# Kernel tuning notes

Measured on AMD Instinct MI355X. Metric: run time of the kernel, lower is better.

The kernel has to match this reference:

```python
import jax, jax.numpy as jnp
import numpy as np

# Module config (matches init_kwargs)
B, H, W, C = 2, 64, 64, 128
NH, K = 4, 7            # num_heads, kernel_size (odd)
HD = C // NH            # head_dim = 32
SCALE = HD ** -0.5


def setup_inputs() -> dict:
    key = jax.random.key(0)
    ks = jax.random.split(key, 5)
    return {
        "x": jax.random.normal(ks[0], (B, H, W, C), jnp.float32),
        "w_qkv": jax.random.normal(ks[1], (C, 3 * C), jnp.float32) * 0.02,
        "b_qkv": jnp.zeros((3 * C,), jnp.float32),
        "rpb": jax.random.normal(ks[2], (NH, 2 * K - 1, 2 * K - 1), jnp.float32) * 0.02,
        "w_proj": jax.random.normal(ks[3], (C, C), jnp.float32) * 0.02,
        "b_proj": jnp.zeros((C,), jnp.float32),
    }


def _window_starts(L):
    # NATTEN clamped window start: max(i-k//2,0), shifted left at right border so the
    # full k-window fits. clip handles both cases since i-k//2 > L-k  <=>  i+k//2 >= L.
    i = jnp.arange(L)
    return jnp.clip(i - K // 2, 0, L - K)  # [L]


def reference(x, w_qkv, b_qkv, rpb, w_proj, b_proj):
    # qkv projection: [B,H,W,3,NH,HD]
    qkv = (x @ w_qkv + b_qkv).reshape(B, H, W, 3, NH, HD)
    q = qkv[..., 0, :, :] * SCALE  # [B,H,W,NH,HD]
    k = qkv[..., 1, :, :]
    v = qkv[..., 2, :, :]

    a = jnp.arange(K)
    idx_h = _window_starts(H)[:, None] + a[None, :]  # [H,K] key rows per query row
    idx_w = _window_starts(W)[:, None] + a[None, :]  # [W,K] key cols per query col

    # Gather k*k neighborhoods (honors the local sparsity; no [HW,HW] matrix):
    # k[:, idx_h] -> [B,H,K,W,NH,HD]; then index W axis -> [B,H,K,W,K,NH,HD]
    k_nb = k[:, idx_h][:, :, :, idx_w]
    v_nb = v[:, idx_h][:, :, :, idx_w]

    # natten2dqkrpb: attn[b,n,i,j,p,q] = <q[b,i,j,n], k[b, ih[i,p], iw[j,q], n]>
    attn = jnp.einsum('bhwnd,bhpwqnd->bnhwpq', q, k_nb)  # [B,NH,H,W,K,K]

    # relative position bias index = (neighbor - query) + (k-1) per axis
    bidx_h = idx_h - jnp.arange(H)[:, None] + (K - 1)  # [H,K] in [0, 2k-2]
    bidx_w = idx_w - jnp.arange(W)[:, None] + (K - 1)  # [W,K]
    bias = rpb[:, bidx_h[:, :, None, None], bidx_w[None, None]]  # [NH,H,K,W,K]
    attn = attn + bias.transpose(0, 1, 3, 2, 4)[None]  # -> [1,NH,H,W,K,K]

    # softmax over the flattened k*k neighborhood
    attn = jax.nn.softmax(attn.reshape(B, NH, H, W, K * K), axis=-1)
    attn = attn.reshape(B, NH, H, W, K, K)

    # natten2dav: weighted sum over neighborhood values
    out = jnp.einsum('bnhwpq,bhpwqnd->bhwnd', attn, v_nb).reshape(B, H, W, C)
    return out @ w_proj + b_proj
```

## Files before the change

### kernel.cpp

```cpp
#include <hip/hip_runtime.h>
#include <hip/hip_bf16.h>
#include <cstddef>

#define BB 2
#define HH 64
#define WW 64
#define SCALE 0.17677669529663687f

#define HALO_H 10
#define HALO_W 14
#define NPIX 140
#define NQ 32

typedef short short8 __attribute__((ext_vector_type(8)));
typedef float f32x4 __attribute__((ext_vector_type(4)));

#if defined(__has_builtin)
#if __has_builtin(__builtin_amdgcn_fdot2_f32_bf16)
#define HAS_BFDOT2 1
#endif
#endif
#ifndef HAS_BFDOT2
#define HAS_BFDOT2 0
#endif

#if HAS_BFDOT2
typedef __bf16 v2bf __attribute__((ext_vector_type(2)));
__device__ inline float bfdot2(uint a, uint b, float c) {
    union { uint u; v2bf v; } ua, ub;
    ua.u = a; ub.u = b;
    return __builtin_amdgcn_fdot2_f32_bf16(ua.v, ub.v, c, false);
}
#endif

__device__ inline ushort f2bf(float f) {
    union { __hip_bfloat16 b; ushort u; } cv;
    cv.b = __float2bfloat16(f);
    return cv.u;
}
__device__ inline float bflo(uint u) { union { uint i; float f; } c; c.i = u << 16; return c.f; }
__device__ inline float bfhi(uint u) { union { uint i; float f; } c; c.i = u & 0xffff0000u; return c.f; }

__global__ __launch_bounds__(256) void qkv_gemm_fused_kernel(
    const float* __restrict__ x, const float* __restrict__ w_qkv,
    const float* __restrict__ b_qkv, const float* __restrict__ w_proj,
    ushort* __restrict__ qkv, ushort* __restrict__ Wp_t)
{
    __shared__ ushort S[64 * 128 + 96 * 128];
    ushort* As = S;
    ushort* Bs = S + 64 * 128;

    const int tid = threadIdx.x;
    const int m0 = blockIdx.x * 64;
    const int n0 = blockIdx.y * 96;

    if (blockIdx.y == 0 && tid < 128)
        Wp_t[(size_t)blockIdx.x * 128 + tid] =
            f2bf(w_proj[(size_t)tid * 128 + blockIdx.x]);

    #pragma unroll
    for (int t = 0; t < 4; ++t) {
        int idx = tid + t * 256;
        int r = idx >> 4, c = idx & 15;
        const float* src = x + (size_t)(m0 + r) * 128 + c * 8;
        float4 v0 = *(const float4*)src;
        float4 v1 = *(const float4*)(src + 4);
        union { ushort s[8]; uint4 q; } u;
        u.s[0] = f2bf(v0.x); u.s[1] = f2bf(v0.y); u.s[2] = f2bf(v0.z); u.s[3] = f2bf(v0.w);
        u.s[4] = f2bf(v1.x); u.s[5] = f2bf(v1.y); u.s[6] = f2bf(v1.z); u.s[7] = f2bf(v1.w);
        *(uint4*)&As[r * 128 + (c ^ (r & 7)) * 8] = u.q;
    }
    #pragma unroll
    for (int t = 0; t < 6; ++t) {
        int idx = tid + t * 256;
        int kc = idx / 96, n = idx - kc * 96;
        union { ushort s[8]; uint4 q; } u;
        #pragma unroll
        for (int e = 0; e < 8; ++e)
            u.s[e] = f2bf(w_qkv[(size_t)(kc * 8 + e) * 384 + n0 + n]);
        *(uint4*)&Bs[n * 128 + ((kc ^ (n & 7)) * 8)] = u.q;
    }
    __syncthreads();

    const int wid = tid >> 6, lane = tid & 63;
    const int l15 = lane & 15, l4 = lane >> 4;
    const int mr = (wid >> 1) * 32, nr = (wid & 1) * 48;

    f32x4 acc[2][3] = {};
    #pragma unroll
    for (int ks = 0; ks < 4; ++ks) {
        short8 af[2], bf[3];
        #pragma unroll
        for (int fm = 0; fm < 2; ++fm) {
            int row = mr + fm * 16 + l15;
            af[fm] = *(const short8*)&As[row * 128 + ((ks * 4 + l4) ^ (row & 7)) * 8];
        }
        #pragma unroll
        for (int fn = 0; fn < 3; ++fn) {
            int row = nr + fn * 16 + l15;
            bf[fn] = *(const short8*)&Bs[row * 128 + ((ks * 4 + l4) ^ (row & 7)) * 8];
        }
        #pragma unroll
        for (int fm = 0; fm < 2; ++fm)
            #pragma unroll
            for (int fn = 0; fn < 3; ++fn)
                acc[fm][fn] = __builtin_amdgcn_mfma_f32_16x16x32_bf16(
                    af[fm], bf[fn], acc[fm][fn], 0, 0, 0);
    }

    __syncthreads();
    ushort* C_s = S;
    #pragma unroll
    for (int fn = 0; fn < 3; ++fn) {
        int colb = nr + fn * 16;
        int col = colb + l15;
        float bc = b_qkv[n0 + col];
        float sc = (n0 + colb < 128) ? SCALE : 1.0f;
        #pragma unroll
        for (int fm = 0; fm < 2; ++fm)
            #pragma unroll
            for (int reg = 0; reg < 4; ++reg) {
                int row = mr + fm * 16 + l4 * 4 + reg;
                C_s[row * 200 + col] = f2bf((acc[fm][fn][reg] + bc) * sc);
            }
    }
    __syncthreads();
    #pragma unroll
    for (int t = 0; t < 3; ++t) {
        int idx = tid + t * 256;
        int row = idx / 12, c = idx - row * 12;
        uint4 v = *(const uint4*)&C_s[row * 200 + c * 8];
        *(uint4*)&qkv[(size_t)(m0 + row) * 384 + n0 + c * 8] = v;
    }
}

__global__ __launch_bounds__(256) void natten_proj_kernel(
    const ushort* __restrict__ qkv,
    const float* __restrict__ rpb,
    const ushort* __restrict__ Wp_t,
    const float* __restrict__ b_proj,
    float* __restrict__ out)
{
    __shared__ ushort KV_s[NPIX * 64];
    __shared__ ushort AO_s[NQ * 128];
    __shared__ float attn_s[NQ * 52];
    __shared__ float rpb_s[676];

    const int tid = threadIdx.x;
    const int bx = ((blockIdx.x & 7) << 5) | (blockIdx.x >> 3);
    const int b  = bx >> 7;
    const int th = (bx >> 3) & 15;
    const int tw = bx & 7;
    const int h0 = th * 4, w0 = tw * 8;
    const int ho = max(0, h0 - 3), wo = max(0, w0 - 3);

    #pragma unroll
    for (int t = 0; t < 3; ++t) {
        int idx = tid + t * 256;
        if (idx < 676) rpb_s[idx] = rpb[idx];
    }

    const int q = tid >> 3, t8 = tid & 7;
    const int qh = h0 + (q >> 3), qw = w0 + (q & 7);
    const int hs = min(max(qh - 3, 0), HH - 7);
    const int ws = min(max(qw - 3, 0), WW - 7);
    const int base_lp = (hs - ho) * HALO_W + (ws - wo);
    const int bh0 = hs - qh + 6, bw0 = ws - qw + 6;
    const size_t qpix = (size_t)((b << 12) + (qh << 6) + qw);

    for (int hd = 0; hd < 4; ++hd) {
        #pragma unroll
        for (int t = 0; t < 5; ++t) {
            int idx = tid + t * 256;
            if (idx < NPIX * 8) {
                int pix = idx >> 3, s = idx & 7;
                int r = pix / HALO_W, c = pix - r * HALO_W;
                int gh = min(ho + r, HH - 1), gw = min(wo + c, WW - 1);
                const ushort* gp = qkv + (size_t)((b << 12) + (gh << 6) + gw) * 384
                                   + 128 + (s >> 2) * 128 + hd * 32 + (s & 3) * 8;
                uint4 v = *(const uint4*)gp;
                int bb = (pix >> 2) & 1;
                int slot = (2 * ((s & 3) ^ (pix & 3)) ^ bb) ^ (s >> 2);
                *(uint4*)&KV_s[pix * 64 + slot * 8] = v;
            }
        }

#if HAS_BFDOT2
        uint4 qb[4];
        #pragma unroll
        for (int d4 = 0; d4 < 4; ++d4)
            qb[d4] = *(const uint4*)(qkv + qpix * 384 + hd * 32 + d4 * 8);
#else
        float qf[32];
        #pragma unroll
        for (int d4 = 0; d4 < 4; ++d4) {
            uint4 qu = *(const uint4*)(qkv + qpix * 384 + hd * 32 + d4 * 8);
            qf[d4*8+0] = bflo(qu.x); qf[d4*8+1] = bfhi(qu.x);
            qf[d4*8+2] = bflo(qu.y); qf[d4*8+3] = bfhi(qu.y);
            qf[d4*8+4] = bflo(qu.z); qf[d4*8+5] = bfhi(qu.z);
            qf[d4*8+6] = bflo(qu.w); qf[d4*8+7] = bfhi(qu.w);
        }
#endif
        __syncthreads();

        float lg[7];
        #pragma unroll
        for (int i = 0; i < 7; ++i) {
            int j = t8 + i * 8;
            float s = -1e30f;
            if (j < 49) {
                int p = (j * 37) >> 8;
                int qq = j - p * 7;
                int lp = base_lp + p * HALO_W + qq;
                int bb = (lp >> 2) & 1;
                float a = 0.f;
                #pragma unroll
                for (int d4 = 0; d4 < 4; ++d4) {
                    uint4 ku = *(const uint4*)&KV_s[lp * 64 + ((2 * (d4 ^ (lp & 3)) ^ bb) * 8)];
#if HAS_BFDOT2
                    a = bfdot2(ku.x, qb[d4].x, a);
                    a = bfdot2(ku.y, qb[d4].y, a);
                    a = bfdot2(ku.z, qb[d4].z, a);
                    a = bfdot2(ku.w, qb[d4].w, a);
#else
                    a += bflo(ku.x)*qf[d4*8+0] + bfhi(ku.x)*qf[d4*8+1]
                       + bflo(ku.y)*qf[d4*8+2] + bfhi(ku.y)*qf[d4*8+3]
                       + bflo(ku.z)*qf[d4*8+4] + bfhi(ku.z)*qf[d4*8+5]
                       + bflo(ku.w)*qf[d4*8+6] + bfhi(ku.w)*qf[d4*8+7];
#endif
                }
                s = a + rpb_s[hd * 169 + (bh0 + p) * 13 + (bw0 + qq)];
            }
            lg[i] = s;
        }

        float m = lg[0];
        #pragma unroll
        for (int i = 1; i < 7; ++i) m = fmaxf(m, lg[i]);
        m = fmaxf(m, __shfl_xor(m, 1));
        m = fmaxf(m, __shfl_xor(m, 2));
        m = fmaxf(m, __shfl_xor(m, 4));
        float ssum = 0.f;
        #pragma unroll
        for (int i = 0; i < 7; ++i) {
            int j = t8 + i * 8;
            lg[i] = (j < 49) ? __expf(lg[i] - m) : 0.f;
            ssum += lg[i];
        }
        ssum += __shfl_xor(ssum, 1);
        ssum += __shfl_xor(ssum, 2);
        ssum += __shfl_xor(ssum, 4);
        float inv = 1.f / ssum;
        #pragma unroll
        for (int i = 0; i < 7; ++i) {
            int j = t8 + i * 8;
            if (j < 49) attn_s[q * 52 + j] = lg[i] * inv;
        }

        const int dd = t8 & 3;
        const int jp = t8 >> 2;
        float o[8] = {};
        #pragma unroll
        for (int i = 0; i < 25; ++i) {
            int j = 2 * i + jp;
            if (j < 49) {
                int p = (j * 37) >> 8;
                int qq = j - p * 7;
                int lp = base_lp + p * HALO_W + qq;
                int bb = (lp >> 2) & 1;
                float a = attn_s[q * 52 + j];
                uint4 vu = *(const uint4*)&KV_s[lp * 64 + (((2 * (dd ^ (lp & 3)) ^ bb) ^ 1) * 8)];
                o[0] += a * bflo(vu.x); o[1] += a * bfhi(vu.x);
                o[2] += a * bflo(vu.y); o[3] += a * bfhi(vu.y);
                o[4] += a * bflo(vu.z); o[5] += a * bfhi(vu.z);
                o[6] += a * bflo(vu.w); o[7] += a * bfhi(vu.w);
            }
        }
        #pragma unroll
        for (int e = 0; e < 8; ++e) o[e] += __shfl_xor(o[e], 4);

        if (t8 < 4) {
            union { ushort s[8]; uint4 u4; } w;
            #pragma unroll
            for (int e = 0; e < 8; ++e) w.s[e] = f2bf(o[e]);
            *(uint4*)&AO_s[q * 128 + (((hd * 4 + dd) ^ (q & 7)) * 8)] = w.u4;
        }
        __syncthreads();
    }

    const int wid = tid >> 6, lane = tid & 63;
    const int l15 = lane & 15, l4 = lane >> 4;
    const int wr = wid >> 1, wc = wid & 1;

    f32x4 pacc[4] = {};
    #pragma unroll
    for (int ks = 0; ks < 4; ++ks) {
        int arow = wr * 16 + l15;
        short8 af = *(const short8*)&AO_s[arow * 128 + ((ks * 4 + l4) ^ (arow & 7)) * 8];
        #pragma unroll
        for (int fn = 0; fn < 4; ++fn) {
            int brow = wc * 64 + fn * 16 + l15;
            short8 bf = *(const short8*)(Wp_t + (size_t)brow * 128 + (ks * 4 + l4) * 8);
            pacc[fn] = __builtin_amdgcn_mfma_f32_16x16x32_bf16(af, bf, pacc[fn], 0, 0, 0);
        }
    }
    #pragma unroll
    for (int fn = 0; fn < 4; ++fn) {
        int col = wc * 64 + fn * 16 + l15;
        float bc = b_proj[col];
        #pragma unroll
        for (int reg = 0; reg < 4; ++reg) {
            int q2 = wr * 16 + l4 * 4 + reg;
            int oh = h0 + (q2 >> 3), ow = w0 + (q2 & 7);
            out[(size_t)((b << 12) + (oh << 6) + ow) * 128 + col] = pacc[fn][reg] + bc;
        }
    }
}

extern "C" void kernel_launch(void* const* d_in, const int* in_sizes, int n_in,
                              void* d_out, int out_size, void* d_ws, size_t ws_size,
                              hipStream_t stream)
{
    const float* x      = (const float*)d_in[0];
    const float* w_qkv  = (const float*)d_in[1];
    const float* b_qkv  = (const float*)d_in[2];
    const float* rpb    = (const float*)d_in[3];
    const float* w_proj = (const float*)d_in[4];
    const float* b_proj = (const float*)d_in[5];
    float* out = (float*)d_out;

    const int M = BB * HH * WW;
    ushort* qkv  = (ushort*)d_ws;
    ushort* Wp_t = qkv + (size_t)M * 384;

    qkv_gemm_fused_kernel<<<dim3(128, 4), 256, 0, stream>>>(
        x, w_qkv, b_qkv, w_proj, qkv, Wp_t);

    natten_proj_kernel<<<256, 256, 0, stream>>>(
        qkv, rpb, Wp_t, b_proj, out);
}
```

Before: 30.33 us.

## Assign one head per wavefront with private K/V tiles, removing per-head block syncs

Replaces the serial loop over four heads, where the whole block reloaded a shared K/V halo and synchronised twice per head, with a layout in which each of the four wavefronts owns one head and its own K/V halo buffer. Each query is now handled by two lanes holding 25 logits in registers, so the attention-probability shared array and its round trip go away, and only one block barrier remains before the projection MFMA. This trades more shared memory (four halo buffers) and much higher register pressure (25 logits plus 32 accumulators per lane) for fewer barriers and more independent loads in flight, which may lower occupancy.

After: 30.34 us. Within noise of the previous version (+0.0%).

```diff
diff --git a/kernel.cpp b/kernel.cpp
--- a/kernel.cpp
+++ b/kernel.cpp
@@ -141,12 +141,13 @@
     const float* __restrict__ b_proj,
     float* __restrict__ out)
 {
-    __shared__ ushort KV_s[NPIX * 64];
+    __shared__ ushort KV_s[4][NPIX * 64];
     __shared__ ushort AO_s[NQ * 128];
-    __shared__ float attn_s[NQ * 52];
     __shared__ float rpb_s[676];
 
     const int tid = threadIdx.x;
+    const int wv = tid >> 6;
+    const int lane = tid & 63;
     const int bx = ((blockIdx.x & 7) << 5) | (blockIdx.x >> 3);
     const int b  = bx >> 7;
     const int th = (bx >> 3) & 15;
@@ -160,7 +161,24 @@
         if (idx < 676) rpb_s[idx] = rpb[idx];
     }
 
-    const int q = tid >> 3, t8 = tid & 7;
+    ushort* KV = &KV_s[wv][0];
+    #pragma unroll
+    for (int t = 0; t < 18; ++t) {
+        int idx = lane + t * 64;
+        if (idx < NPIX * 8) {
+            int pix = idx >> 3, s = idx & 7;
+            int r = pix / HALO_W, c = pix - r * HALO_W;
+            int gh = min(ho + r, HH - 1), gw = min(wo + c, WW - 1);
+            const ushort* gp = qkv + (size_t)((b << 12) + (gh << 6) + gw) * 384
+                               + 128 + (s >> 2) * 128 + wv * 32 + (s & 3) * 8;
+            uint4 v = *(const uint4*)gp;
+            int bb = (pix >> 2) & 1;
+            int slot = (2 * ((s & 3) ^ (pix & 3)) ^ bb) ^ (s >> 2);
+            *(uint4*)&KV[pix * 64 + slot * 8] = v;
+        }
+    }
+
+    const int q = lane >> 1, half = lane & 1;
     const int qh = h0 + (q >> 3), qw = w0 + (q & 7);
     const int hs = min(max(qh - 3, 0), HH - 7);
     const int ws = min(max(qw - 3, 0), WW - 7);
@@ -168,129 +186,106 @@
     const int bh0 = hs - qh + 6, bw0 = ws - qw + 6;
     const size_t qpix = (size_t)((b << 12) + (qh << 6) + qw);
 
-    for (int hd = 0; hd < 4; ++hd) {
-        #pragma unroll
-        for (int t = 0; t < 5; ++t) {
-            int idx = tid + t * 256;
-            if (idx < NPIX * 8) {
-                int pix = idx >> 3, s = idx & 7;
-                int r = pix / HALO_W, c = pix - r * HALO_W;
-                int gh = min(ho + r, HH - 1), gw = min(wo + c, WW - 1);
-                const ushort* gp = qkv + (size_t)((b << 12) + (gh << 6) + gw) * 384
-                                   + 128 + (s >> 2) * 128 + hd * 32 + (s & 3) * 8;
-                uint4 v = *(const uint4*)gp;
-                int bb = (pix >> 2) & 1;
-                int slot = (2 * ((s & 3) ^ (pix & 3)) ^ bb) ^ (s >> 2);
-                *(uint4*)&KV_s[pix * 64 + slot * 8] = v;
+#if HAS_BFDOT2
+    uint4 qb[4];
+    #pragma unroll
+    for (int d4 = 0; d4 < 4; ++d4)
+        qb[d4] = *(const uint4*)(qkv + qpix * 384 + wv * 32 + d4 * 8);
+#else
+    float qf[32];
+    #pragma unroll
+    for (int d4 = 0; d4 < 4; ++d4) {
+        uint4 qu = *(const uint4*)(qkv + qpix * 384 + wv * 32 + d4 * 8);
+        qf[d4*8+0] = bflo(qu.x); qf[d4*8+1] = bfhi(qu.x);
+        qf[d4*8+2] = bflo(qu.y); qf[d4*8+3] = bfhi(qu.y);
+        qf[d4*8+4] = bflo(qu.z); qf[d4*8+5] = bfhi(qu.z);
+        qf[d4*8+6] = bflo(qu.w); qf[d4*8+7] = bfhi(qu.w);
+    }
+#endif
+    __syncthreads();
+
+    float lg[25];
+    #pragma unroll
+    for (int i = 0; i < 25; ++i) {
+        int j = half + 2 * i;
+        float s = -1e30f;
+        if (j < 49) {
+            int p = (j * 37) >> 8;
+            int qq = j - p * 7;
+            int lp = base_lp + p * HALO_W + qq;
+            int bb = (lp >> 2) & 1;
+            float a = 0.f;
+            #pragma unroll
+            for (int d4 = 0; d4 < 4; ++d4) {
+                uint4 ku = *(const uint4*)&KV[lp * 64 + ((2 * (d4 ^ (lp & 3)) ^ bb) * 8)];
+#if HAS_BFDOT2
+                a = bfdot2(ku.x, qb[d4].x, a);
+                a = bfdot2(ku.y, qb[d4].y, a);
+                a = bfdot2(ku.z, qb[d4].z, a);
+                a = bfdot2(ku.w, qb[d4].w, a);
+#else
+                a += bflo(ku.x)*qf[d4*8+0] + bfhi(ku.x)*qf[d4*8+1]
+                   + bflo(ku.y)*qf[d4*8+2] + bfhi(ku.y)*qf[d4*8+3]
+                   + bflo(ku.z)*qf[d4*8+4] + bfhi(ku.z)*qf[d4*8+5]
+                   + bflo(ku.w)*qf[d4*8+6] + bfhi(ku.w)*qf[d4*8+7];
+#endif
             }
-        }
-
-#if HAS_BFDOT2
-        uint4 qb[4];
-        #pragma unroll
-        for (int d4 = 0; d4 < 4; ++d4)
-            qb[d4] = *(const uint4*)(qkv + qpix * 384 + hd * 32 + d4 * 8);
-#else
-        float qf[32];
-        #pragma unroll
-        for (int d4 = 0; d4 < 4; ++d4) {
-            uint4 qu = *(const uint4*)(qkv + qpix * 384 + hd * 32 + d4 * 8);
-            qf[d4*8+0] = bflo(qu.x); qf[d4*8+1] = bfhi(qu.x);
-            qf[d4*8+2] = bflo(qu.y); qf[d4*8+3] = bfhi(qu.y);
-            qf[d4*8+4] = bflo(qu.z); qf[d4*8+5] = bfhi(qu.z);
-            qf[d4*8+6] = bflo(qu.w); qf[d4*8+7] = bfhi(qu.w);
-        }
-#endif
-        __syncthreads();
-
-        float lg[7];
-        #pragma unroll
-        for (int i = 0; i < 7; ++i) {
-            int j = t8 + i * 8;
-            float s = -1e30f;
-            if (j < 49) {
-                int p = (j * 37) >> 8;
-                int qq = j - p * 7;
-                int lp = base_lp + p * HALO_W + qq;
-                int bb = (lp >> 2) & 1;
-                float a = 0.f;
-                #pragma unroll
-                for (int d4 = 0; d4 < 4; ++d4) {
-                    uint4 ku = *(const uint4*)&KV_s[lp * 64 + ((2 * (d4 ^ (lp & 3)) ^ bb) * 8)];
-#if HAS_BFDOT2
-                    a = bfdot2(ku.x, qb[d4].x, a);
-                    a = bfdot2(ku.y, qb[d4].y, a);
-                    a = bfdot2(ku.z, qb[d4].z, a);
-                    a = bfdot2(ku.w, qb[d4].w, a);
-#else
-                    a += bflo(ku.x)*qf[d4*8+0] + bfhi(ku.x)*qf[d4*8+1]
-                       + bflo(ku.y)*qf[d4*8+2] + bfhi(ku.y)*qf[d4*8+3]
-                       + bflo(ku.z)*qf[d4*8+4] + bfhi(ku.z)*qf[d4*8+5]
-                       + bflo(ku.w)*qf[d4*8+6] + bfhi(ku.w)*qf[d4*8+7];
-#endif
-                }
-                s = a + rpb_s[hd * 169 + (bh0 + p) * 13 + (bw0 + qq)];
+            s = a + rpb_s[wv * 169 + (bh0 + p) * 13 + (bw0 + qq)];
+        }
+        lg[i] = s;
+    }
+
+    float m = lg[0];
+    #pragma unroll
+    for (int i = 1; i < 25; ++i) m = fmaxf(m, lg[i]);
+    m = fmaxf(m, __shfl_xor(m, 1));
+    float ssum = 0.f;
+    #pragma unroll
+    for (int i = 0; i < 25; ++i) {
+        int j = half + 2 * i;
+        lg[i] = (j < 49) ? __expf(lg[i] - m) : 0.f;
+        ssum += lg[i];
+    }
+    ssum += __shfl_xor(ssum, 1);
+    float inv = 1.f / ssum;
+    #pragma unroll
+    for (int i = 0; i < 25; ++i) lg[i] *= inv;
+
+    float o[32] = {};
+    #pragma unroll
+    for (int i = 0; i < 25; ++i) {
+        int j = half + 2 * i;
+        if (j < 49) {
+            int p = (j * 37) >> 8;
+            int qq = j - p * 7;
+            int lp = base_lp + p * HALO_W + qq;
+            int bb = (lp >> 2) & 1;
+            float a = lg[i];
+            #pragma unroll
+            for (int d4 = 0; d4 < 4; ++d4) {
+                uint4 vu = *(const uint4*)&KV[lp * 64 + (((2 * (d4 ^ (lp & 3)) ^ bb) ^ 1) * 8)];
+                o[d4*8+0] += a * bflo(vu.x); o[d4*8+1] += a * bfhi(vu.x);
+                o[d4*8+2] += a * bflo(vu.y); o[d4*8+3] += a * bfhi(vu.y);
+                o[d4*8+4] += a * bflo(vu.z); o[d4*8+5] += a * bfhi(vu.z);
+                o[d4*8+6] += a * bflo(vu.w); o[d4*8+7] += a * bfhi(vu.w);
             }
-            lg[i] = s;
-        }
-
-        float m = lg[0];
-        #pragma unroll
-        for (int i = 1; i < 7; ++i) m = fmaxf(m, lg[i]);
-        m = fmaxf(m, __shfl_xor(m, 1));
-        m = fmaxf(m, __shfl_xor(m, 2));
-        m = fmaxf(m, __shfl_xor(m, 4));
-        float ssum = 0.f;
-        #pragma unroll
-        for (int i = 0; i < 7; ++i) {
-            int j = t8 + i * 8;
-            lg[i] = (j < 49) ? __expf(lg[i] - m) : 0.f;
-            ssum += lg[i];
-        }
-        ssum += __shfl_xor(ssum, 1);
-        ssum += __shfl_xor(ssum, 2);
-        ssum += __shfl_xor(ssum, 4);
-        float inv = 1.f / ssum;
-        #pragma unroll
-        for (int i = 0; i < 7; ++i) {
-            int j = t8 + i * 8;
-            if (j < 49) attn_s[q * 52 + j] = lg[i] * inv;
-        }
-
-        const int dd = t8 & 3;
-        const int jp = t8 >> 2;
-        float o[8] = {};
-        #pragma unroll
-        for (int i = 0; i < 25; ++i) {
-            int j = 2 * i + jp;
-            if (j < 49) {
-                int p = (j * 37) >> 8;
-                int qq = j - p * 7;
-                int lp = base_lp + p * HALO_W + qq;
-                int bb = (lp >> 2) & 1;
-                float a = attn_s[q * 52 + j];
-                uint4 vu = *(const uint4*)&KV_s[lp * 64 + (((2 * (dd ^ (lp & 3)) ^ bb) ^ 1) * 8)];
-                o[0] += a * bflo(vu.x); o[1] += a * bfhi(vu.x);
-                o[2] += a * bflo(vu.y); o[3] += a * bfhi(vu.y);
-                o[4] += a * bflo(vu.z); o[5] += a * bfhi(vu.z);
-                o[6] += a * bflo(vu.w); o[7] += a * bfhi(vu.w);
-            }
-        }
-        #pragma unroll
-        for (int e = 0; e < 8; ++e) o[e] += __shfl_xor(o[e], 4);
-
-        if (t8 < 4) {
-            union { ushort s[8]; uint4 u4; } w;
-            #pragma unroll
-            for (int e = 0; e < 8; ++e) w.s[e] = f2bf(o[e]);
-            *(uint4*)&AO_s[q * 128 + (((hd * 4 + dd) ^ (q & 7)) * 8)] = w.u4;
-        }
-        __syncthreads();
-    }
-
-    const int wid = tid >> 6, lane = tid & 63;
+        }
+    }
+    #pragma unroll
+    for (int e = 0; e < 32; ++e) o[e] += __shfl_xor(o[e], 1);
+
+    #pragma unroll
+    for (int cc = 0; cc < 2; ++cc) {
+        int d4 = half * 2 + cc;
+        union { ushort s[8]; uint4 u4; } w;
+        #pragma unroll
+        for (int e = 0; e < 8; ++e) w.s[e] = f2bf(o[d4 * 8 + e]);
+        *(uint4*)&AO_s[q * 128 + (((wv * 4 + d4) ^ (q & 7)) * 8)] = w.u4;
+    }
+    __syncthreads();
+
     const int l15 = lane & 15, l4 = lane >> 4;
-    const int wr = wid >> 1, wc = wid & 1;
+    const int wr = wv >> 1, wc = wv & 1;
 
     f32x4 pacc[4] = {};
     #pragma unroll
```
